# Performance work log

Hardware: AMD Instinct MI355X
Metric: run time of the kernel (lower is better)

The kernel has to match this reference:

```python
import jax, jax.numpy as jnp
import numpy as np

B, NL, L1, D = 16, 12, 197, 768   # batch, num_layers, 1+num_patches, embed_dim
E, K, C, IMG = 4, 3, 21, 224      # num_experts, topk, num_classes, image_size


def setup_inputs() -> dict:
    key = jax.random.key(0)
    k0, k1, k2 = jax.random.split(key, 3)
    features = jax.random.normal(k0, (B, NL, L1, D), jnp.float32)
    gate_W = jax.random.normal(k1, (D, E), jnp.float32) / np.sqrt(D).astype(np.float32)
    gate_b = jnp.zeros((E,), jnp.float32)
    expert_W = jax.random.normal(k2, (E, D, C), jnp.float32) / np.sqrt(D).astype(np.float32)
    expert_b = jnp.zeros((E, C), jnp.float32)
    return dict(features=features, gate_W=gate_W, gate_b=gate_b,
                expert_W=expert_W, expert_b=expert_b)


def reference(features, gate_W, gate_b, expert_W, expert_b):
    cls_tokens = features[:, :, 0, :]          # [B, NL, D]
    feats = features[:, :, 1:, :]              # [B, NL, L, D]
    gate_score = cls_tokens @ gate_W + gate_b  # [B, NL, E]
    gate_prob = jax.nn.softmax(gate_score.transpose(0, 2, 1), axis=-1)  # [B, E, NL]
    # per-expert topk over layers (vectorized over experts)
    topv, topi = jax.lax.top_k(gate_prob, K)   # [B, E, K]
    # gather selected layer feature maps: [B, E, K, L, D]
    gathered = jnp.take_along_axis(feats[:, None], topi[:, :, :, None, None], axis=2)
    w = jax.nn.softmax(topv, axis=-1)          # re-softmax of topk values, [B, E, K]
    mixed = jnp.einsum('bek,bekld->beld', w, gathered)  # [B, E, L, D]
    # expert heads (UPerNet modeled as linear decode + bilinear upsample)
    logits = jnp.einsum('beld,edc->belc', mixed, expert_W) + expert_b[None, :, None, :]
    L = logits.shape[2]
    g = int(np.sqrt(L))                        # 14x14 patch grid
    logits = logits.reshape(B, E, g, g, C).transpose(0, 1, 4, 2, 3)  # [B,E,C,g,g]
    logits = jax.image.resize(logits, (B, E, C, IMG, IMG), method='bilinear')
    return logits.mean(axis=1)                 # mean over experts -> [B, C, IMG, IMG]
```

## Files before the change

### kernel.cpp

```cpp
#include <hip/hip_runtime.h>
#include <math.h>

#define B_ 16
#define NL_ 12
#define L1_ 197
#define D_ 768
#define E_ 4
#define K_ 3
#define C_ 21
#define IMG_ 224
#define LP_ 196
#define NJ_ 84
#define MT_ 52
#define KSTEPS 24

typedef __attribute__((ext_vector_type(8))) short short8;
typedef __attribute__((ext_vector_type(4))) float f32x4;
typedef unsigned short ushort_t;

__device__ __forceinline__ ushort_t bf16rne(float x) {
    unsigned u = __float_as_uint(x);
    unsigned r = (u + 0x7FFFu + ((u >> 16) & 1u)) >> 16;
    return (ushort_t)r;
}

__device__ __forceinline__ void select_be(const float* __restrict__ gs, int b, int e,
                                          int idx[3], float w[3]) {
    float p[NL_]; float mx = -1e30f;
    #pragma unroll
    for (int nl = 0; nl < NL_; ++nl) { float v = gs[(b * NL_ + nl) * E_ + e]; p[nl] = v; mx = fmaxf(mx, v); }
    float ss = 0.f;
    #pragma unroll
    for (int nl = 0; nl < NL_; ++nl) { p[nl] = expf(p[nl] - mx); ss += p[nl]; }
    float inv = 1.0f / ss;
    #pragma unroll
    for (int nl = 0; nl < NL_; ++nl) p[nl] *= inv;
    unsigned used = 0; float v[3];
    #pragma unroll
    for (int k = 0; k < 3; ++k) {
        float best = -1.f; int bi = 0;
        #pragma unroll
        for (int nl = 0; nl < NL_; ++nl)
            if (!((used >> nl) & 1u) && p[nl] > best) { best = p[nl]; bi = nl; }
        used |= 1u << bi; idx[k] = bi; v[k] = best;
    }
    float x1 = expf(v[1] - v[0]), x2 = expf(v[2] - v[0]);
    float isw = 1.0f / (1.0f + x1 + x2);
    w[0] = isw; w[1] = x1 * isw; w[2] = x2 * isw;
}

__global__ __launch_bounds__(256) void prep_kernel(
        const float* __restrict__ feat, const float* __restrict__ gW,
        const float* __restrict__ gb, const float* __restrict__ eW,
        ushort_t* __restrict__ WtB, float* __restrict__ gs) {
    int blk = blockIdx.x, t = threadIdx.x;
    if (blk < B_ * NL_) {
        if (t < 64) {
            const float* cls = feat + (size_t)blk * L1_ * D_;
            float a0 = 0.f, a1 = 0.f, a2 = 0.f, a3 = 0.f;
            for (int q = 0; q < D_ / 64; ++q) {
                int d = t + 64 * q;
                float x = cls[d];
                float4 w = *(const float4*)(gW + (size_t)d * E_);
                a0 += x * w.x; a1 += x * w.y; a2 += x * w.z; a3 += x * w.w;
            }
            for (int off = 32; off > 0; off >>= 1) {
                a0 += __shfl_down(a0, off); a1 += __shfl_down(a1, off);
                a2 += __shfl_down(a2, off); a3 += __shfl_down(a3, off);
            }
            if (t == 0) {
                gs[blk * E_ + 0] = a0 + gb[0]; gs[blk * E_ + 1] = a1 + gb[1];
                gs[blk * E_ + 2] = a2 + gb[2]; gs[blk * E_ + 3] = a3 + gb[3];
            }
        }
    } else {
        int j = blk - B_ * NL_;
        if (j < NJ_) {
            int e = j / C_, c = j % C_;
            for (int k = t; k < D_; k += 256)
                WtB[(size_t)j * D_ + k] = bf16rne(eW[((size_t)e * D_ + k) * C_ + c]);
        } else {
            for (int k = t; k < D_; k += 256) WtB[(size_t)j * D_ + k] = 0;
        }
    }
}

__global__ __launch_bounds__(256) void select_kernel(
        const float* __restrict__ gs, int* __restrict__ topi,
        float* __restrict__ wgt, int* __restrict__ flag) {
    __shared__ int sidx[B_ * E_ * 3];
    int t = threadIdx.x;
    if (t < B_ * E_) {
        int b = t >> 2, e = t & 3;
        int idx[3]; float w[3];
        select_be(gs, b, e, idx, w);
        #pragma unroll
        for (int k = 0; k < 3; ++k) {
            topi[t * 3 + k] = idx[k]; wgt[t * 3 + k] = w[k]; sidx[t * 3 + k] = idx[k];
        }
    }
    __syncthreads();
    if (t < B_ * NL_) {
        int b = t / NL_, nl = t % NL_;
        int f = 0;
        #pragma unroll
        for (int ek = 0; ek < 12; ++ek) f |= (sidx[b * 12 + ek] == nl);
        flag[t] = f;
    }
}

__global__ __launch_bounds__(256, 3) void gemm_kernel(
        const float* __restrict__ feat, const ushort_t* __restrict__ WtB,
        const int* __restrict__ flag, float* __restrict__ proj) {
    int blk = blockIdx.x;
    int tile = blk & 3;
    int bn = blk >> 2;
    if (flag[bn] == 0) return;
    int rows_real = min(MT_, LP_ - tile * MT_);

    __shared__ short8 Ab[2][64 * 5];
    __shared__ short8 Bb[2][96 * 5];

    int t = threadIdx.x;
    int w = t >> 6, lane = t & 63;
    int r = t >> 2, kg = t & 3;
    int aslotw = kg ^ (r & 3);
    bool avalid = r < rows_real;
    bool bvalid1 = t < 128;

    const float* arow_base = feat + ((size_t)bn * L1_ + 1 + tile * MT_ + r) * D_;
    const ushort_t* brow0 = WtB + (size_t)r * D_;
    const ushort_t* brow1 = WtB + (size_t)(64 + r) * D_;

    int arow = w * 16 + (lane & 15);
    int aidx = arow * 5 + ((lane >> 4) ^ (arow & 3));
    int bidx[6];
    #pragma unroll
    for (int nt = 0; nt < 6; ++nt) {
        int jr = nt * 16 + (lane & 15);
        bidx[nt] = jr * 5 + ((lane >> 4) ^ (jr & 3));
    }

    {
        f32x4 fa0 = {0,0,0,0}, fa1 = {0,0,0,0};
        if (avalid) { const f32x4* p = (const f32x4*)(arow_base); fa0 = p[kg*2]; fa1 = p[kg*2+1]; }
        short8 av;
        #pragma unroll
        for (int i = 0; i < 4; ++i) { av[i] = (short)bf16rne(fa0[i]); av[i+4] = (short)bf16rne(fa1[i]); }
        Ab[0][r * 5 + aslotw] = av;
        Bb[0][r * 5 + aslotw] = *(const short8*)(brow0 + kg * 8);
        if (bvalid1) Bb[0][(64 + r) * 5 + aslotw] = *(const short8*)(brow1 + kg * 8);
    }
    __syncthreads();

    f32x4 acc[6];
    #pragma unroll
    for (int nt = 0; nt < 6; ++nt) acc[nt] = (f32x4)0.0f;

    for (int s = 0; s < KSTEPS; ++s) {
        int cur = s & 1;
        f32x4 fa0 = {0,0,0,0}, fa1 = {0,0,0,0};
        short8 wb0, wb1;
        if (s + 1 < KSTEPS) {
            int k0 = (s + 1) * 32;
            if (avalid) { const f32x4* p = (const f32x4*)(arow_base + k0); fa0 = p[kg*2]; fa1 = p[kg*2+1]; }
            wb0 = *(const short8*)(brow0 + k0 + kg * 8);
            if (bvalid1) wb1 = *(const short8*)(brow1 + k0 + kg * 8);
        }
        short8 af = Ab[cur][aidx];
        #pragma unroll
        for (int nt = 0; nt < 6; ++nt)
            acc[nt] = __builtin_amdgcn_mfma_f32_16x16x32_bf16(af, Bb[cur][bidx[nt]], acc[nt], 0, 0, 0);
        if (s + 1 < KSTEPS) {
            int nb = cur ^ 1;
            short8 av;
            #pragma unroll
            for (int i = 0; i < 4; ++i) { av[i] = (short)bf16rne(fa0[i]); av[i+4] = (short)bf16rne(fa1[i]); }
            Ab[nb][r * 5 + aslotw] = av;
            Bb[nb][r * 5 + aslotw] = wb0;
            if (bvalid1) Bb[nb][(64 + r) * 5 + aslotw] = wb1;
        }
        __syncthreads();
    }

    int lr = w * 16 + ((lane >> 4) << 2);
    int l0 = tile * MT_ + lr;
    if (lr < MT_ && l0 < LP_) {
        #pragma unroll
        for (int nt = 0; nt < 6; ++nt) {
            int j = nt * 16 + (lane & 15);
            if (j < NJ_)
                *(f32x4*)(proj + ((size_t)bn * NJ_ + j) * LP_ + l0) = acc[nt];
        }
    }
}

__global__ __launch_bounds__(256) void upsample_kernel(
        const float* __restrict__ proj, const int* __restrict__ topi,
        const float* __restrict__ wgt, const float* __restrict__ eb,
        float* __restrict__ out) {
    int bq = blockIdx.x;
    int q = bq & 3;
    int bc = bq >> 2;
    int b = bc / C_, c = bc % C_;
    int t = threadIdx.x;
    __shared__ float s[LP_];
    if (t < LP_) {
        float a = 0.25f * (eb[c] + eb[C_ + c] + eb[2 * C_ + c] + eb[3 * C_ + c]);
        #pragma unroll
        for (int e = 0; e < E_; ++e) {
            int base = (b * E_ + e) * 3;
            #pragma unroll
            for (int k = 0; k < 3; ++k) {
                int nl = topi[base + k];
                float wv = 0.25f * wgt[base + k];
                a += wv * proj[(((size_t)b * NL_ + nl) * NJ_ + e * C_ + c) * LP_ + t];
            }
        }
        s[t] = a;
    }
    __syncthreads();
    float4* out4 = (float4*)out + (size_t)bc * IMG_ * (IMG_ / 4);
    for (int i = t; i < 56 * 56; i += 256) {
        int oy = q * 56 + i / 56;
        int ox4 = (i % 56) * 4;
        float fy = (oy + 0.5f) * 0.0625f - 0.5f;
        fy = fminf(fmaxf(fy, 0.0f), 13.0f);
        int y0 = (int)fy;
        float ty = fy - (float)y0;
        int y1 = min(y0 + 1, 13);
        const float* r0 = s + y0 * 14;
        const float* r1 = s + y1 * 14;
        float4 res;
        float* rp = (float*)&res;
        for (int u = 0; u < 4; ++u) {
            int ox = ox4 + u;
            float fx = (ox + 0.5f) * 0.0625f - 0.5f;
            fx = fminf(fmaxf(fx, 0.0f), 13.0f);
            int x0 = (int)fx;
            float tx = fx - (float)x0;
            int x1 = min(x0 + 1, 13);
            float v00 = r0[x0], v01 = r0[x1];
            float v10 = r1[x0], v11 = r1[x1];
            float top = v00 + tx * (v01 - v00);
            float bot = v10 + tx * (v11 - v10);
            rp[u] = top + ty * (bot - top);
        }
        out4[oy * 56 + (i % 56)] = res;
    }
}

extern "C" void kernel_launch(void* const* d_in, const int* in_sizes, int n_in,
                              void* d_out, int out_size, void* d_ws, size_t ws_size,
                              hipStream_t stream) {
    const float* feat = (const float*)d_in[0];
    const float* gW   = (const float*)d_in[1];
    const float* gb   = (const float*)d_in[2];
    const float* eW   = (const float*)d_in[3];
    const float* eb   = (const float*)d_in[4];
    float* out = (float*)d_out;

    float* ws = (float*)d_ws;
    float*    gs   = ws;
    int*      topi = (int*)(ws + 768);
    float*    wgt  = ws + 960;
    int*      flag = (int*)(ws + 1152);
    ushort_t* WtB  = (ushort_t*)(ws + 1536);
    float*    proj = ws + 38400;

    hipLaunchKernelGGL(prep_kernel, dim3(B_ * NL_ + 96), dim3(256), 0, stream,
                       feat, gW, gb, eW, WtB, gs);
    hipLaunchKernelGGL(select_kernel, dim3(1), dim3(256), 0, stream,
                       gs, topi, wgt, flag);
    hipLaunchKernelGGL(gemm_kernel, dim3(B_ * NL_ * 4), dim3(256), 0, stream,
                       feat, WtB, flag, proj);
    hipLaunchKernelGGL(upsample_kernel, dim3(B_ * C_ * 4), dim3(256), 0, stream,
                       proj, topi, wgt, eb, out);
}
```

Measured before the change: 52.86 us.

## Split GEMM K dimension across blocks, compact selected layers, load A directly to registers

The GEMM now splits the reduction dimension into two halves handled by separate blocks, writing two partial projection buffers that the upsample kernel sums. The select kernel builds a compacted list of selected (batch, layer) pairs, so GEMM blocks map densely onto real work instead of exiting early on a flag. The A operand is loaded straight from global memory into MFMA register layout with a 3-deep register prefetch, dropping the A shared-memory tile and using lighter barriers. This doubles the number of blocks and adds partial-sum traffic and a second proj buffer read in exchange for more parallelism and less LDS work.

```diff
diff --git a/kernel.cpp b/kernel.cpp
--- a/kernel.cpp
+++ b/kernel.cpp
@@ -13,6 +13,8 @@
 #define NJ_ 84
 #define MT_ 52
 #define KSTEPS 24
+#define KHS 12
+#define PROJ_SZ ((size_t)B_ * NL_ * NJ_ * LP_)
 
 typedef __attribute__((ext_vector_type(8))) short short8;
 typedef __attribute__((ext_vector_type(4))) float f32x4;
@@ -87,8 +89,9 @@
 
 __global__ __launch_bounds__(256) void select_kernel(
         const float* __restrict__ gs, int* __restrict__ topi,
-        float* __restrict__ wgt, int* __restrict__ flag) {
+        float* __restrict__ wgt, int* __restrict__ list, int* __restrict__ nsel) {
     __shared__ int sidx[B_ * E_ * 3];
+    __shared__ int sflag[B_ * NL_];
     int t = threadIdx.x;
     if (t < B_ * E_) {
         int b = t >> 2, e = t & 3;
@@ -105,92 +108,118 @@
         int f = 0;
         #pragma unroll
         for (int ek = 0; ek < 12; ++ek) f |= (sidx[b * 12 + ek] == nl);
-        flag[t] = f;
-    }
-}
-
-__global__ __launch_bounds__(256, 3) void gemm_kernel(
+        sflag[t] = f;
+    }
+    __syncthreads();
+    if (t == 0) {
+        int n = 0;
+        for (int bn = 0; bn < B_ * NL_; ++bn)
+            if (sflag[bn]) list[n++] = bn;
+        nsel[0] = n;
+    }
+}
+
+__global__ __launch_bounds__(256) void gemm_kernel(
         const float* __restrict__ feat, const ushort_t* __restrict__ WtB,
-        const int* __restrict__ flag, float* __restrict__ proj) {
+        const int* __restrict__ list, const int* __restrict__ nsel,
+        float* __restrict__ proj) {
     int blk = blockIdx.x;
-    int tile = blk & 3;
-    int bn = blk >> 2;
-    if (flag[bn] == 0) return;
-    int rows_real = min(MT_, LP_ - tile * MT_);
-
-    __shared__ short8 Ab[2][64 * 5];
+    if (blk >= nsel[0] * 8) return;
+    int kh = blk & 1;
+    int tile = (blk >> 1) & 3;
+    int bn = list[blk >> 3];
+
     __shared__ short8 Bb[2][96 * 5];
 
     int t = threadIdx.x;
     int w = t >> 6, lane = t & 63;
     int r = t >> 2, kg = t & 3;
     int aslotw = kg ^ (r & 3);
-    bool avalid = r < rows_real;
     bool bvalid1 = t < 128;
 
-    const float* arow_base = feat + ((size_t)bn * L1_ + 1 + tile * MT_ + r) * D_;
     const ushort_t* brow0 = WtB + (size_t)r * D_;
     const ushort_t* brow1 = WtB + (size_t)(64 + r) * D_;
 
-    int arow = w * 16 + (lane & 15);
-    int aidx = arow * 5 + ((lane >> 4) ^ (arow & 3));
+    int la = lane & 15, kp = lane >> 4;
+    int arow = tile * MT_ + w * 16 + la;
+    arow = min(arow, LP_ - 1);
+    const float* aptr = feat + ((size_t)bn * L1_ + 1 + arow) * D_ + kp * 8;
+
     int bidx[6];
     #pragma unroll
     for (int nt = 0; nt < 6; ++nt) {
-        int jr = nt * 16 + (lane & 15);
-        bidx[nt] = jr * 5 + ((lane >> 4) ^ (jr & 3));
-    }
-
+        int jr = nt * 16 + la;
+        bidx[nt] = jr * 5 + (kp ^ (jr & 3));
+    }
+
+    const int kbase = kh * KHS * 32;
+    #define AK(s) (kbase + (s) * 32)
+
+    f32x4 A0[3], A1[3];
+    A0[0] = *(const f32x4*)(aptr + AK(0));
+    A1[0] = *(const f32x4*)(aptr + AK(0) + 4);
+    A0[1] = *(const f32x4*)(aptr + AK(1));
+    A1[1] = *(const f32x4*)(aptr + AK(1) + 4);
     {
-        f32x4 fa0 = {0,0,0,0}, fa1 = {0,0,0,0};
-        if (avalid) { const f32x4* p = (const f32x4*)(arow_base); fa0 = p[kg*2]; fa1 = p[kg*2+1]; }
-        short8 av;
-        #pragma unroll
-        for (int i = 0; i < 4; ++i) { av[i] = (short)bf16rne(fa0[i]); av[i+4] = (short)bf16rne(fa1[i]); }
-        Ab[0][r * 5 + aslotw] = av;
-        Bb[0][r * 5 + aslotw] = *(const short8*)(brow0 + kg * 8);
-        if (bvalid1) Bb[0][(64 + r) * 5 + aslotw] = *(const short8*)(brow1 + kg * 8);
-    }
-    __syncthreads();
+        short8 wb0 = *(const short8*)(brow0 + AK(0) + kg * 8);
+        Bb[0][r * 5 + aslotw] = wb0;
+        if (bvalid1) {
+            short8 wb1 = *(const short8*)(brow1 + AK(0) + kg * 8);
+            Bb[0][(64 + r) * 5 + aslotw] = wb1;
+        }
+    }
+    asm volatile("s_waitcnt lgkmcnt(0)" ::: "memory");
+    __builtin_amdgcn_s_barrier();
+    __builtin_amdgcn_sched_barrier(0);
 
     f32x4 acc[6];
     #pragma unroll
     for (int nt = 0; nt < 6; ++nt) acc[nt] = (f32x4)0.0f;
 
-    for (int s = 0; s < KSTEPS; ++s) {
+    #pragma unroll
+    for (int s = 0; s < KHS; ++s) {
         int cur = s & 1;
-        f32x4 fa0 = {0,0,0,0}, fa1 = {0,0,0,0};
+        if (s + 2 < KHS) {
+            A0[(s + 2) % 3] = *(const f32x4*)(aptr + AK(s + 2));
+            A1[(s + 2) % 3] = *(const f32x4*)(aptr + AK(s + 2) + 4);
+        }
         short8 wb0, wb1;
-        if (s + 1 < KSTEPS) {
-            int k0 = (s + 1) * 32;
-            if (avalid) { const f32x4* p = (const f32x4*)(arow_base + k0); fa0 = p[kg*2]; fa1 = p[kg*2+1]; }
-            wb0 = *(const short8*)(brow0 + k0 + kg * 8);
-            if (bvalid1) wb1 = *(const short8*)(brow1 + k0 + kg * 8);
-        }
-        short8 af = Ab[cur][aidx];
-        #pragma unroll
-        for (int nt = 0; nt < 6; ++nt)
-            acc[nt] = __builtin_amdgcn_mfma_f32_16x16x32_bf16(af, Bb[cur][bidx[nt]], acc[nt], 0, 0, 0);
-        if (s + 1 < KSTEPS) {
-            int nb = cur ^ 1;
-            short8 av;
+        if (s + 1 < KHS) {
+            wb0 = *(const short8*)(brow0 + AK(s + 1) + kg * 8);
+            if (bvalid1) wb1 = *(const short8*)(brow1 + AK(s + 1) + kg * 8);
+        }
+        {
+            f32x4 c0 = A0[s % 3], c1 = A1[s % 3];
+            short8 af;
             #pragma unroll
-            for (int i = 0; i < 4; ++i) { av[i] = (short)bf16rne(fa0[i]); av[i+4] = (short)bf16rne(fa1[i]); }
-            Ab[nb][r * 5 + aslotw] = av;
-            Bb[nb][r * 5 + aslotw] = wb0;
-            if (bvalid1) Bb[nb][(64 + r) * 5 + aslotw] = wb1;
-        }
-        __syncthreads();
-    }
-
-    int lr = w * 16 + ((lane >> 4) << 2);
+            for (int i = 0; i < 4; ++i) {
+                af[i]     = (short)bf16rne(c0[i]);
+                af[i + 4] = (short)bf16rne(c1[i]);
+            }
+            #pragma unroll
+            for (int nt = 0; nt < 6; ++nt)
+                acc[nt] = __builtin_amdgcn_mfma_f32_16x16x32_bf16(
+                    af, Bb[cur][bidx[nt]], acc[nt], 0, 0, 0);
+        }
+        if (s + 1 < KHS) {
+            Bb[cur ^ 1][r * 5 + aslotw] = wb0;
+            if (bvalid1) Bb[cur ^ 1][(64 + r) * 5 + aslotw] = wb1;
+        }
+        asm volatile("s_waitcnt lgkmcnt(0)" ::: "memory");
+        __builtin_amdgcn_s_barrier();
+        __builtin_amdgcn_sched_barrier(0);
+    }
+    #undef AK
+
+    int lr = w * 16 + (kp << 2);
     int l0 = tile * MT_ + lr;
     if (lr < MT_ && l0 < LP_) {
+        float* projh = proj + kh * PROJ_SZ;
         #pragma unroll
         for (int nt = 0; nt < 6; ++nt) {
-            int j = nt * 16 + (lane & 15);
+            int j = nt * 16 + la;
             if (j < NJ_)
-                *(f32x4*)(proj + ((size_t)bn * NJ_ + j) * LP_ + l0) = acc[nt];
+                *(f32x4*)(projh + ((size_t)bn * NJ_ + j) * LP_ + l0) = acc[nt];
         }
     }
 }
@@ -214,7 +243,8 @@
             for (int k = 0; k < 3; ++k) {
                 int nl = topi[base + k];
                 float wv = 0.25f * wgt[base + k];
-                a += wv * proj[(((size_t)b * NL_ + nl) * NJ_ + e * C_ + c) * LP_ + t];
+                size_t off = (((size_t)b * NL_ + nl) * NJ_ + e * C_ + c) * LP_ + t;
+                a += wv * (proj[off] + proj[off + PROJ_SZ]);
             }
         }
         s[t] = a;
@@ -264,16 +294,17 @@
     float*    gs   = ws;
     int*      topi = (int*)(ws + 768);
     float*    wgt  = ws + 960;
-    int*      flag = (int*)(ws + 1152);
+    int*      list = (int*)(ws + 1152);
+    int*      nsel = (int*)(ws + 1344);
     ushort_t* WtB  = (ushort_t*)(ws + 1536);
     float*    proj = ws + 38400;
 
     hipLaunchKernelGGL(prep_kernel, dim3(B_ * NL_ + 96), dim3(256), 0, stream,
                        feat, gW, gb, eW, WtB, gs);
     hipLaunchKernelGGL(select_kernel, dim3(1), dim3(256), 0, stream,
-                       gs, topi, wgt, flag);
-    hipLaunchKernelGGL(gemm_kernel, dim3(B_ * NL_ * 4), dim3(256), 0, stream,
-                       feat, WtB, flag, proj);
+                       gs, topi, wgt, list, nsel);
+    hipLaunchKernelGGL(gemm_kernel, dim3(B_ * NL_ * 4 * 2), dim3(256), 0, stream,
+                       feat, WtB, list, nsel, proj);
     hipLaunchKernelGGL(upsample_kernel, dim3(B_ * C_ * 4), dim3(256), 0, stream,
                        proj, topi, wgt, eb, out);
 }
```

New measurement: 67.68 us. +28.0%, slower.
